# Optimization experiments

Hardware: AMD Instinct MI355X
Metric: run time of the kernel (lower is better)

Reference implementation:

```python
import jax, jax.numpy as jnp
import numpy as np
import math

BASE = 10000
N_HEADS = 16


def _rope_cos_sin(seq_len, head_dim, dtype=jnp.float32):
    # thetas = base ** (-2 * (arange(hd//2) / hd))
    thetas = BASE ** (-2.0 * (jnp.arange(head_dim // 2, dtype=jnp.float32) / head_dim))
    freqs = jnp.arange(seq_len, dtype=jnp.float32)[:, None] * thetas[None, :]  # [S, hd/2]
    return jnp.cos(freqs).astype(dtype), jnp.sin(freqs).astype(dtype)


def _apply_rope(x, cos, sin):
    # x: [B, H, S, D]; complex multiply on consecutive (even, odd) pairs
    b, h, s, d = x.shape
    xr = x.reshape(b, h, s, d // 2, 2)
    x0, x1 = xr[..., 0], xr[..., 1]
    c = cos[None, None, :, :]
    sn = sin[None, None, :, :]
    o0 = x0 * c - x1 * sn
    o1 = x0 * sn + x1 * c
    return jnp.stack([o0, o1], axis=-1).reshape(b, h, s, d)


def setup_inputs() -> dict:
    key = jax.random.key(0)
    k1, k2, k3 = jax.random.split(key, 3)
    B, S, E = 2, 2048, 1024
    x = jax.random.normal(k1, (B, S, E), dtype=jnp.float32)
    W_qkv = jax.random.normal(k2, (3 * E, E), dtype=jnp.float32) * (1.0 / math.sqrt(E))
    W_o = jax.random.normal(k3, (E, E), dtype=jnp.float32) * (1.0 / math.sqrt(E))
    return {"x": x, "W_qkv": W_qkv, "W_o": W_o}


def reference(x, W_qkv, W_o):
    B, S, E = x.shape
    H = N_HEADS
    D = E // H
    qkv = x @ W_qkv.T  # [B, S, 3E]
    q, k, v = jnp.split(qkv, 3, axis=-1)
    # [B, S, E] -> [B, H, S, D]
    q = q.reshape(B, S, H, D).transpose(0, 2, 1, 3)
    k = k.reshape(B, S, H, D).transpose(0, 2, 1, 3)
    v = v.reshape(B, S, H, D).transpose(0, 2, 1, 3)
    cos, sin = _rope_cos_sin(S, D)
    q = _apply_rope(q, cos, sin)
    k = _apply_rope(k, cos, sin)
    scores = jnp.einsum("bhqd,bhkd->bhqk", q, k) / math.sqrt(D)
    causal = jnp.tril(jnp.ones((S, S), dtype=bool))
    scores = jnp.where(causal[None, None, :, :], scores, -jnp.inf)
    wts = jax.nn.softmax(scores, axis=-1)
    y = jnp.einsum("bhqk,bhkd->bhqd", wts, v)
    y = y.transpose(0, 2, 1, 3).reshape(B, S, E)
    return y @ W_o.T
```

## Files before the change

### kernel.cpp

```cpp
#include <hip/hip_runtime.h>
#include <math.h>
#include <stdint.h>

typedef __bf16 bf16;
typedef __bf16 bf16x4 __attribute__((ext_vector_type(4)));
typedef __bf16 bf16x8 __attribute__((ext_vector_type(8)));
typedef float  f32x4  __attribute__((ext_vector_type(4)));

#define QSCALE 0.18033688011112042f

#define XB_OFF    ((size_t)0)
#define WQKV_OFF  ((size_t)8388608)
#define WO_OFF    ((size_t)14680064)
#define QB_OFF    ((size_t)16777216)
#define KB_OFF    ((size_t)25165824)
#define VT_OFF    ((size_t)33554432)
#define YB_OFF    ((size_t)41943040)
#define COS_OFF   ((size_t)50331648)
#define SIN_OFF   ((size_t)50593792)

__device__ __forceinline__ void gload_lds16(const void* g, void* l) {
  __builtin_amdgcn_global_load_lds((const __attribute__((address_space(1))) void*)g,
                                   (__attribute__((address_space(3))) void*)l,
                                   16, 0, 0);
}

__global__ void cvt_all(const float* __restrict__ x, const float* __restrict__ wqkv,
                        const float* __restrict__ wo, bf16* __restrict__ Xb,
                        bf16* __restrict__ Wqkvb, bf16* __restrict__ Wob,
                        float* __restrict__ cosT, float* __restrict__ sinT) {
  const int bid = blockIdx.x;
  if (bid >= 8192) {
    int i = (bid - 8192) * 256 + threadIdx.x;
    int s = i >> 5, f = i & 31;
    float theta = exp2f(-(float)f * (13.287712379549449f / 32.0f));
    float ang = (float)s * theta;
    cosT[i] = cosf(ang);
    sinT[i] = sinf(ang);
    return;
  }
  int i = bid * 256 + threadIdx.x;
  const float* src; bf16* dst; int off;
  if (i < 1048576)      { src = x;    dst = Xb;    off = i; }
  else if (i < 1835008) { src = wqkv; dst = Wqkvb; off = i - 1048576; }
  else                  { src = wo;   dst = Wob;   off = i - 1835008; }
  float4 v = ((const float4*)src)[off];
  bf16x4 o = {(bf16)v.x, (bf16)v.y, (bf16)v.z, (bf16)v.w};
  *(bf16x4*)(dst + (size_t)off * 4) = o;
}

template <int EPI, int NJ>
__global__ __launch_bounds__(256) void gemm_nt(
    const bf16* __restrict__ A, const bf16* __restrict__ Bw, float* __restrict__ Cout,
    bf16* __restrict__ Qb, bf16* __restrict__ Kb, bf16* __restrict__ Vt,
    const float* __restrict__ cosT, const float* __restrict__ sinT,
    int M, int N, int K)
{
  constexpr int BN  = NJ * 32;
  constexpr int ASZ = 128 * 64;
  constexpr int BSZ = BN * 64;
  __shared__ bf16 smem[ASZ + BSZ];
  bf16* sA = smem;
  bf16* sB = smem + ASZ;

  const int tid  = threadIdx.x;
  const int w    = tid >> 6;
  const int lane = tid & 63;
  const int quad = lane >> 4;
  const int l16  = lane & 15;
  const int wm   = (w >> 1) * 64;
  const int wn   = (w & 1) * (NJ * 16);
  const int tm   = blockIdx.y * 128;
  const int tn   = blockIdx.x * BN;
  const int srow = lane >> 3;
  const int scol = ((lane & 7) ^ srow) << 3;
  const int rsw  = l16 & 7;

  f32x4 zero4 = {0.f, 0.f, 0.f, 0.f};
  f32x4 acc[4][NJ];
#pragma unroll
  for (int i = 0; i < 4; ++i)
#pragma unroll
    for (int j = 0; j < NJ; ++j) acc[i][j] = zero4;

  const bf16* Abase = A + (size_t)tm * K;
  const bf16* Bbase = Bw + (size_t)tn * K;

  for (int k0 = 0; k0 < K; k0 += 64) {
#pragma unroll
    for (int c = 0; c < 4; ++c) {
      const int rb = (w * 4 + c) * 8;
      gload_lds16(Abase + (size_t)(rb + srow) * K + (k0 + scol), &sA[rb * 64]);
    }
#pragma unroll
    for (int c = 0; c < BN / 32; ++c) {
      const int rb = (w * (BN / 32) + c) * 8;
      gload_lds16(Bbase + (size_t)(rb + srow) * K + (k0 + scol), &sB[rb * 64]);
    }
    __syncthreads();
#pragma unroll
    for (int kk = 0; kk < 2; ++kk) {
      bf16x8 af[4], bfr[NJ];
#pragma unroll
      for (int i = 0; i < 4; ++i)
        af[i] = *(const bf16x8*)&sA[(wm + i * 16 + l16) * 64 + (((kk * 4 + quad) ^ rsw) << 3)];
#pragma unroll
      for (int j = 0; j < NJ; ++j)
        bfr[j] = *(const bf16x8*)&sB[(wn + j * 16 + l16) * 64 + (((kk * 4 + quad) ^ rsw) << 3)];
#pragma unroll
      for (int i = 0; i < 4; ++i)
#pragma unroll
        for (int j = 0; j < NJ; ++j)
          acc[i][j] = __builtin_amdgcn_mfma_f32_16x16x32_bf16(af[i], bfr[j], acc[i][j], 0, 0, 0);
    }
    __syncthreads();
  }

  if constexpr (EPI == 0) {
#pragma unroll
    for (int i = 0; i < 4; ++i) {
      const int rowb = wm + i * 16 + quad * 4;
#pragma unroll
      for (int j = 0; j < 4; ++j) {
        const int col = wn + j * 16 + l16;
        const int ch = col >> 3, cl = col & 7;
#pragma unroll
        for (int r = 0; r < 4; ++r) {
          const int row = rowb + r;
          const int key = (row >> 2) & 7;
          const int ph = (ch & 8) | ((ch ^ key) & 7);
          smem[row * 128 + ph * 8 + cl] = (bf16)acc[i][j][r];
        }
      }
    }
    __syncthreads();
    const int row  = tid >> 1;
    const int half = tid & 1;
    const int m = tm + row;
    const int b = m >> 11, s = m & 2047;
    const int key = (row >> 2) & 7;
    if (tn >= 2048) {
      const int h = ((tn - 2048) >> 6) + half;
      bf16* vdst = Vt + ((size_t)((b << 4) + h) * 64) * 2048 + s;
#pragma unroll
      for (int c = 0; c < 8; ++c) {
        const int ch = half * 8 + c;
        const int ph = (ch & 8) | ((ch ^ key) & 7);
        bf16x8 v = *(const bf16x8*)&smem[row * 128 + ph * 8];
#pragma unroll
        for (int t = 0; t < 8; ++t)
          vdst[(size_t)(c * 8 + t) * 2048] = v[t];
      }
    } else {
      const int nbase = tn + half * 64;
      const int g = nbase >> 10;
      const int h = (nbase & 1023) >> 6;
      bf16* dst = (g == 0) ? Qb : Kb;
      const size_t obase = ((size_t)((b << 4) + h) * 2048 + s) * 64;
#pragma unroll
      for (int c = 0; c < 8; ++c) {
        const int ch = half * 8 + c;
        const int ph = (ch & 8) | ((ch ^ key) & 7);
        bf16x8 v = *(const bf16x8*)&smem[row * 128 + ph * 8];
        f32x4 c4 = *(const f32x4*)&cosT[s * 32 + c * 4];
        f32x4 s4 = *(const f32x4*)&sinT[s * 32 + c * 4];
        bf16x8 ov;
#pragma unroll
        for (int t = 0; t < 4; ++t) {
          float x0 = (float)v[2 * t], x1 = (float)v[2 * t + 1];
          float o0 = x0 * c4[t] - x1 * s4[t];
          float o1 = x0 * s4[t] + x1 * c4[t];
          if (g == 0) { o0 *= QSCALE; o1 *= QSCALE; }
          ov[2 * t] = (bf16)o0;
          ov[2 * t + 1] = (bf16)o1;
        }
        *(bf16x8*)&dst[obase + c * 8] = ov;
      }
    }
  } else {
#pragma unroll
    for (int i = 0; i < 4; ++i)
#pragma unroll
      for (int j = 0; j < NJ; ++j)
#pragma unroll
        for (int r = 0; r < 4; ++r) {
          const int m = tm + wm + i * 16 + quad * 4 + r;
          const int n = tn + wn + j * 16 + l16;
          Cout[(size_t)m * N + n] = acc[i][j][r];
        }
  }
}

__global__ __launch_bounds__(256) void attn_fwd(
    const bf16* __restrict__ Qb, const bf16* __restrict__ Kb,
    const bf16* __restrict__ Vt, bf16* __restrict__ Yb)
{
  __shared__ bf16 sK[2][64 * 64];
  __shared__ bf16 sV[2][64 * 64];
  __shared__ bf16 sP[64 * 68];

  const int bh  = blockIdx.x;
  const int y   = blockIdx.y;
  const int npass = (y >= 16) ? 2 : 1;
  const int tid = threadIdx.x;
  const int w    = tid >> 6;
  const int lane = tid & 63;
  const int quad = lane >> 4;
  const int l16  = lane & 15;

  const size_t head = (size_t)bh * 2048 * 64;
  const bf16* khead = Kb + head;
  const bf16* vhead = Vt + head;

  const int srow = lane >> 3;
  const int scol = ((lane & 7) ^ srow) << 3;
  const int rs   = l16 & 7;
  const int cb0  = (quad ^ rs) << 3;
  const int cb1  = ((quad + 4) ^ rs) << 3;

  f32x4 zero4 = {0.f, 0.f, 0.f, 0.f};
  const bf16 one = (bf16)1.0f;
  const bf16x8 bones = {one, one, one, one, one, one, one, one};
  const int b = bh >> 4, h = bh & 15;
  const int prow = (w * 16 + l16) * 68;

  auto stage = [&](int kt, int bsel) {
    const bf16* ks = khead + (size_t)kt * 4096;
    const bf16* vs = vhead + kt * 64;
#pragma unroll
    for (int c = 0; c < 2; ++c) {
      const int chunk = (w << 1) + c;
      const int row = (chunk << 3) + srow;
      gload_lds16(ks + row * 64 + scol,           &sK[bsel][chunk * 512]);
      gload_lds16(vs + (size_t)row * 2048 + scol, &sV[bsel][chunk * 512]);
    }
  };

  for (int pass = 0; pass < npass; ++pass) {
    const int qt = pass ? (y - 16) : (31 - y);
    const int nk = qt + 1;

    const bf16* qsrc = Qb + head + (size_t)qt * 4096;
    bf16x8 bq0 = *(const bf16x8*)&qsrc[(w * 16 + l16) * 64 + quad * 8];
    bf16x8 bq1 = *(const bf16x8*)&qsrc[(w * 16 + l16) * 64 + 32 + quad * 8];

    f32x4 o[4] = {zero4, zero4, zero4, zero4};
    f32x4 acc_li = zero4;
    const int qpos = qt * 64 + w * 16 + l16;

    __syncthreads();
    stage(0, 0);

    for (int kt = 0; kt < nk; ++kt) {
      __syncthreads();
      if (kt + 1 < nk) stage(kt + 1, (kt + 1) & 1);

      const bf16* bK = sK[kt & 1];
      const bf16* bV = sV[kt & 1];

      f32x4 sv[4];
#pragma unroll
      for (int i = 0; i < 4; ++i) {
        const int m = i * 16 + l16;
        bf16x8 k0 = *(const bf16x8*)&bK[m * 64 + cb0];
        bf16x8 k1 = *(const bf16x8*)&bK[m * 64 + cb1];
        f32x4 cacc = zero4;
        cacc = __builtin_amdgcn_mfma_f32_16x16x32_bf16(k0, bq0, cacc, 0, 0, 0);
        cacc = __builtin_amdgcn_mfma_f32_16x16x32_bf16(k1, bq1, cacc, 0, 0, 0);
        sv[i] = cacc;
      }

      if (kt == qt) {
#pragma unroll
        for (int i = 0; i < 4; ++i) {
          int kbase = kt * 64 + i * 16 + quad * 4;
#pragma unroll
          for (int r = 0; r < 4; ++r)
            sv[i][r] = (kbase + r > qpos) ? -3.0e38f : sv[i][r];
        }
      }

      float pv[4][4];
#pragma unroll
      for (int i = 0; i < 4; ++i)
#pragma unroll
        for (int r = 0; r < 4; ++r)
          pv[i][r] = exp2f(sv[i][r]);

#pragma unroll
      for (int i = 0; i < 4; ++i) {
        bf16x4 pk = {(bf16)pv[i][0], (bf16)pv[i][1], (bf16)pv[i][2], (bf16)pv[i][3]};
        *(bf16x4*)&sP[prow + i * 16 + quad * 4] = pk;
      }
      bf16x8 ap0 = *(const bf16x8*)&sP[prow + quad * 8];
      bf16x8 ap1 = *(const bf16x8*)&sP[prow + 32 + quad * 8];

      acc_li = __builtin_amdgcn_mfma_f32_16x16x32_bf16(ap0, bones, acc_li, 0, 0, 0);
      acc_li = __builtin_amdgcn_mfma_f32_16x16x32_bf16(ap1, bones, acc_li, 0, 0, 0);

#pragma unroll
      for (int i = 0; i < 4; ++i) {
        const int m = i * 16 + l16;
        bf16x8 v0 = *(const bf16x8*)&bV[m * 64 + cb0];
        bf16x8 v1 = *(const bf16x8*)&bV[m * 64 + cb1];
        o[i] = __builtin_amdgcn_mfma_f32_16x16x32_bf16(ap0, v0, o[i], 0, 0, 0);
        o[i] = __builtin_amdgcn_mfma_f32_16x16x32_bf16(ap1, v1, o[i], 0, 0, 0);
      }
    }

#pragma unroll
    for (int r = 0; r < 4; ++r) {
      float inv = 1.0f / acc_li[r];
      int s = qt * 64 + w * 16 + quad * 4 + r;
      size_t base = ((size_t)(b * 2048 + s)) * 1024 + h * 64;
#pragma unroll
      for (int i = 0; i < 4; ++i)
        Yb[base + i * 16 + l16] = (bf16)(o[i][r] * inv);
    }
  }
}

extern "C" void kernel_launch(void* const* d_in, const int* in_sizes, int n_in,
                              void* d_out, int out_size, void* d_ws, size_t ws_size,
                              hipStream_t stream) {
  (void)in_sizes; (void)n_in; (void)out_size; (void)ws_size;
  const float* x    = (const float*)d_in[0];
  const float* wqkv = (const float*)d_in[1];
  const float* wo   = (const float*)d_in[2];
  float* out = (float*)d_out;
  char* ws = (char*)d_ws;

  bf16* Xb    = (bf16*)(ws + XB_OFF);
  bf16* Wqkvb = (bf16*)(ws + WQKV_OFF);
  bf16* Wob   = (bf16*)(ws + WO_OFF);
  bf16* Qb    = (bf16*)(ws + QB_OFF);
  bf16* Kb    = (bf16*)(ws + KB_OFF);
  bf16* Vtb   = (bf16*)(ws + VT_OFF);
  bf16* Yb    = (bf16*)(ws + YB_OFF);
  float* cosT = (float*)(ws + COS_OFF);
  float* sinT = (float*)(ws + SIN_OFF);

  cvt_all<<<8448, 256, 0, stream>>>(x, wqkv, wo, Xb, Wqkvb, Wob, cosT, sinT);

  gemm_nt<0, 4><<<dim3(24, 32), 256, 0, stream>>>(Xb, Wqkvb, nullptr, Qb, Kb, Vtb,
                                                  cosT, sinT, 4096, 3072, 1024);
  attn_fwd<<<dim3(32, 24), 256, 0, stream>>>(Qb, Kb, Vtb, Yb);
  gemm_nt<1, 2><<<dim3(16, 32), 256, 0, stream>>>(Yb, Wob, out, nullptr, nullptr, nullptr,
                                                  nullptr, nullptr, 4096, 1024, 1024);
}
```

Measured before the change: 176.1 us.

## Stage K in 128-row pairs in LDS and load V directly from global

The attention kernel now stages two 64-row K tiles per LDS buffer, which halves the barrier count per key tile. V is no longer staged in LDS; each lane reads its V fragments straight from global memory into registers, and those loads are issued before the QK^T MFMAs. Launch bounds now request 3 blocks per CU. The goal is fewer syncs and less LDS traffic, at the cost of uncoalesced strided global reads of V (row stride 2048) and more register pressure.

```diff
diff --git a/kernel.cpp b/kernel.cpp
--- a/kernel.cpp
+++ b/kernel.cpp
@@ -191,12 +191,11 @@
   }
 }
 
-__global__ __launch_bounds__(256) void attn_fwd(
+__global__ __launch_bounds__(256, 3) void attn_fwd(
     const bf16* __restrict__ Qb, const bf16* __restrict__ Kb,
     const bf16* __restrict__ Vt, bf16* __restrict__ Yb)
 {
-  __shared__ bf16 sK[2][64 * 64];
-  __shared__ bf16 sV[2][64 * 64];
+  __shared__ bf16 sK[2][128 * 64];
   __shared__ bf16 sP[64 * 68];
 
   const int bh  = blockIdx.x;
@@ -224,21 +223,20 @@
   const int b = bh >> 4, h = bh & 15;
   const int prow = (w * 16 + l16) * 68;
 
-  auto stage = [&](int kt, int bsel) {
-    const bf16* ks = khead + (size_t)kt * 4096;
-    const bf16* vs = vhead + kt * 64;
-#pragma unroll
-    for (int c = 0; c < 2; ++c) {
-      const int chunk = (w << 1) + c;
+  auto stage_pair = [&](int pr, int bsel) {
+    const bf16* ks = khead + (size_t)pr * 8192;
+#pragma unroll
+    for (int c = 0; c < 4; ++c) {
+      const int chunk = w * 4 + c;
       const int row = (chunk << 3) + srow;
-      gload_lds16(ks + row * 64 + scol,           &sK[bsel][chunk * 512]);
-      gload_lds16(vs + (size_t)row * 2048 + scol, &sV[bsel][chunk * 512]);
+      gload_lds16(ks + row * 64 + scol, &sK[bsel][chunk * 512]);
     }
   };
 
   for (int pass = 0; pass < npass; ++pass) {
     const int qt = pass ? (y - 16) : (31 - y);
     const int nk = qt + 1;
+    const int np = (nk + 1) >> 1;
 
     const bf16* qsrc = Qb + head + (size_t)qt * 4096;
     bf16x8 bq0 = *(const bf16x8*)&qsrc[(w * 16 + l16) * 64 + quad * 8];
@@ -249,62 +247,73 @@
     const int qpos = qt * 64 + w * 16 + l16;
 
     __syncthreads();
-    stage(0, 0);
-
-    for (int kt = 0; kt < nk; ++kt) {
+    stage_pair(0, 0);
+
+    for (int pr = 0; pr < np; ++pr) {
       __syncthreads();
-      if (kt + 1 < nk) stage(kt + 1, (kt + 1) & 1);
-
-      const bf16* bK = sK[kt & 1];
-      const bf16* bV = sV[kt & 1];
-
-      f32x4 sv[4];
-#pragma unroll
-      for (int i = 0; i < 4; ++i) {
-        const int m = i * 16 + l16;
-        bf16x8 k0 = *(const bf16x8*)&bK[m * 64 + cb0];
-        bf16x8 k1 = *(const bf16x8*)&bK[m * 64 + cb1];
-        f32x4 cacc = zero4;
-        cacc = __builtin_amdgcn_mfma_f32_16x16x32_bf16(k0, bq0, cacc, 0, 0, 0);
-        cacc = __builtin_amdgcn_mfma_f32_16x16x32_bf16(k1, bq1, cacc, 0, 0, 0);
-        sv[i] = cacc;
-      }
-
-      if (kt == qt) {
-#pragma unroll
-        for (int i = 0; i < 4; ++i) {
-          int kbase = kt * 64 + i * 16 + quad * 4;
-#pragma unroll
-          for (int r = 0; r < 4; ++r)
-            sv[i][r] = (kbase + r > qpos) ? -3.0e38f : sv[i][r];
+      if (pr + 1 < np) stage_pair(pr + 1, (pr + 1) & 1);
+
+      const bf16* bK = sK[pr & 1];
+
+#pragma unroll
+      for (int sub = 0; sub < 2; ++sub) {
+        const int kt = pr * 2 + sub;
+        if (kt < nk) {
+          const bf16* vb = vhead + kt * 64;
+          bf16x8 v0[4], v1[4];
+#pragma unroll
+          for (int i = 0; i < 4; ++i) {
+            const int m = i * 16 + l16;
+            v0[i] = *(const bf16x8*)&vb[(size_t)m * 2048 + quad * 8];
+            v1[i] = *(const bf16x8*)&vb[(size_t)m * 2048 + 32 + quad * 8];
+          }
+
+          f32x4 sv[4];
+#pragma unroll
+          for (int i = 0; i < 4; ++i) {
+            const int m = i * 16 + l16;
+            bf16x8 k0 = *(const bf16x8*)&bK[sub * 4096 + m * 64 + cb0];
+            bf16x8 k1 = *(const bf16x8*)&bK[sub * 4096 + m * 64 + cb1];
+            f32x4 cacc = zero4;
+            cacc = __builtin_amdgcn_mfma_f32_16x16x32_bf16(k0, bq0, cacc, 0, 0, 0);
+            cacc = __builtin_amdgcn_mfma_f32_16x16x32_bf16(k1, bq1, cacc, 0, 0, 0);
+            sv[i] = cacc;
+          }
+
+          if (kt == qt) {
+#pragma unroll
+            for (int i = 0; i < 4; ++i) {
+              int kbase = kt * 64 + i * 16 + quad * 4;
+#pragma unroll
+              for (int r = 0; r < 4; ++r)
+                sv[i][r] = (kbase + r > qpos) ? -3.0e38f : sv[i][r];
+            }
+          }
+
+          float pv[4][4];
+#pragma unroll
+          for (int i = 0; i < 4; ++i)
+#pragma unroll
+            for (int r = 0; r < 4; ++r)
+              pv[i][r] = exp2f(sv[i][r]);
+
+#pragma unroll
+          for (int i = 0; i < 4; ++i) {
+            bf16x4 pk = {(bf16)pv[i][0], (bf16)pv[i][1], (bf16)pv[i][2], (bf16)pv[i][3]};
+            *(bf16x4*)&sP[prow + i * 16 + quad * 4] = pk;
+          }
+          bf16x8 ap0 = *(const bf16x8*)&sP[prow + quad * 8];
+          bf16x8 ap1 = *(const bf16x8*)&sP[prow + 32 + quad * 8];
+
+          acc_li = __builtin_amdgcn_mfma_f32_16x16x32_bf16(ap0, bones, acc_li, 0, 0, 0);
+          acc_li = __builtin_amdgcn_mfma_f32_16x16x32_bf16(ap1, bones, acc_li, 0, 0, 0);
+
+#pragma unroll
+          for (int i = 0; i < 4; ++i) {
+            o[i] = __builtin_amdgcn_mfma_f32_16x16x32_bf16(ap0, v0[i], o[i], 0, 0, 0);
+            o[i] = __builtin_amdgcn_mfma_f32_16x16x32_bf16(ap1, v1[i], o[i], 0, 0, 0);
+          }
         }
-      }
-
-      float pv[4][4];
-#pragma unroll
-      for (int i = 0; i < 4; ++i)
-#pragma unroll
-        for (int r = 0; r < 4; ++r)
-          pv[i][r] = exp2f(sv[i][r]);
-
-#pragma unroll
-      for (int i = 0; i < 4; ++i) {
-        bf16x4 pk = {(bf16)pv[i][0], (bf16)pv[i][1], (bf16)pv[i][2], (bf16)pv[i][3]};
-        *(bf16x4*)&sP[prow + i * 16 + quad * 4] = pk;
-      }
-      bf16x8 ap0 = *(const bf16x8*)&sP[prow + quad * 8];
-      bf16x8 ap1 = *(const bf16x8*)&sP[prow + 32 + quad * 8];
-
-      acc_li = __builtin_amdgcn_mfma_f32_16x16x32_bf16(ap0, bones, acc_li, 0, 0, 0);
-      acc_li = __builtin_amdgcn_mfma_f32_16x16x32_bf16(ap1, bones, acc_li, 0, 0, 0);
-
-#pragma unroll
-      for (int i = 0; i < 4; ++i) {
-        const int m = i * 16 + l16;
-        bf16x8 v0 = *(const bf16x8*)&bV[m * 64 + cb0];
-        bf16x8 v1 = *(const bf16x8*)&bV[m * 64 + cb1];
-        o[i] = __builtin_amdgcn_mfma_f32_16x16x32_bf16(ap0, v0, o[i], 0, 0, 0);
-        o[i] = __builtin_amdgcn_mfma_f32_16x16x32_bf16(ap1, v1, o[i], 0, 0, 0);
       }
     }
 
```

Result: slower. 212.2 us (+20.5%).
